# Kernel tuning notes

Measured on AMD Instinct MI355X. Metric: run time of the kernel, lower is better.

## Reference

```python
import jax, jax.numpy as jnp
import numpy as np

NUM_GROUPS = 32
EPS = 1e-6


def group_norm(x, gamma, beta):
    # x: (B, C, H, W), 32 groups, eps=1e-6, affine
    B, C, H, W = x.shape
    xg = x.reshape(B, NUM_GROUPS, C // NUM_GROUPS, H, W)
    mean = xg.mean(axis=(2, 3, 4), keepdims=True)
    var = xg.var(axis=(2, 3, 4), keepdims=True)
    xn = ((xg - mean) * jax.lax.rsqrt(var + EPS)).reshape(B, C, H, W)
    return xn * gamma[None, :, None, None] + beta[None, :, None, None]


def conv1x1(x, w, b):
    # 1x1 conv == channel matmul. x: (B,C,H,W), w: (O,C), b: (O,)
    return jnp.einsum('bchw,oc->bohw', x, w) + b[None, :, None, None]


def setup_inputs() -> dict:
    key = jax.random.key(0)
    B, C, H, W = 16, 512, 32, 32
    ks = jax.random.split(key, 12)
    s = 1.0 / np.sqrt(C)
    return {
        'x': jax.random.normal(ks[0], (B, C, H, W), dtype=jnp.float32),
        'gn_gamma': jnp.ones((C,), dtype=jnp.float32),
        'gn_beta': jnp.zeros((C,), dtype=jnp.float32),
        'wq': jax.random.normal(ks[1], (C, C), dtype=jnp.float32) * s,
        'bq': jnp.zeros((C,), dtype=jnp.float32),
        'wk': jax.random.normal(ks[2], (C, C), dtype=jnp.float32) * s,
        'bk': jnp.zeros((C,), dtype=jnp.float32),
        'wv': jax.random.normal(ks[3], (C, C), dtype=jnp.float32) * s,
        'bv': jnp.zeros((C,), dtype=jnp.float32),
        'wp': jax.random.normal(ks[4], (C, C), dtype=jnp.float32) * s,
        'bp': jnp.zeros((C,), dtype=jnp.float32),
    }


def reference(x, gn_gamma, gn_beta, wq, bq, wk, bk, wv, bv, wp, bp):
    B, C, H, W = x.shape
    residual = x
    xn = group_norm(x, gn_gamma, gn_beta)
    q = conv1x1(xn, wq, bq).reshape(B, C, H * W)  # (B, C, HW)
    k = conv1x1(xn, wk, bk).reshape(B, C, H * W)
    v = conv1x1(xn, wv, bv).reshape(B, C, H * W)
    scale = C ** (-0.5)
    # energy[b,i,j] = q_i . k_j
    energy = jnp.einsum('bci,bcj->bij', q, k) * scale
    attn = jax.nn.softmax(energy, axis=-1)
    # out[b,c,i] = sum_j attn[b,i,j] * v[b,c,j]
    out = jnp.einsum('bij,bcj->bci', attn, v).reshape(B, C, H, W)
    out = conv1x1(out, wp, bp)
    return out + residual
```

## Files before the change

### kernel.cpp

```cpp
#include <hip/hip_runtime.h>
#include <hip/hip_bf16.h>

using bf16 = __hip_bfloat16;

typedef __attribute__((ext_vector_type(8))) __bf16 bf16x8;
typedef __attribute__((ext_vector_type(4))) float floatx4;

#define EPS 1e-6f

#define RAW_BARRIER()  asm volatile("s_barrier" ::: "memory")
#define WAIT_VM6()     asm volatile("s_waitcnt vmcnt(6)" ::: "memory")
#define WAIT_VM4()     asm volatile("s_waitcnt vmcnt(4)" ::: "memory")
#define WAIT_VM0()     asm volatile("s_waitcnt vmcnt(0)" ::: "memory")

__device__ __forceinline__ void load_lds16(const void* g, void* l) {
    __builtin_amdgcn_global_load_lds(
        (const __attribute__((address_space(1))) void*)g,
        (__attribute__((address_space(3))) void*)l, 16, 0, 0);
}

__device__ __forceinline__ void storeOut(float* p, float v) { *p = v; }
__device__ __forceinline__ void storeOut(bf16* p, float v) { *p = __float2bfloat16(v); }

template <int BM, int BIAS_MODE, int SCALE_EN, int RESID_EN, int EXP_MODE,
          int ROWDIV, int QKV, typename OutT>
__global__ __launch_bounds__(256, 2) void gemm_nt(
    const bf16* __restrict__ A, long long aStride, int lda,
    const bf16* __restrict__ B, long long bStride, int ldb,
    OutT* __restrict__ D, long long dStride, int ldd,
    bf16* __restrict__ vout, long long vStride,
    const float* __restrict__ bias,
    const float* __restrict__ resid, long long rStride, int ldr,
    float* __restrict__ rowsum, int rsStride,
    int K, float scale, int tpb, int gx)
{
    constexpr int MI = BM / 32;
    constexpr int NLA = BM / 64;
    constexpr int NL = NLA + 2;

    __shared__ bf16 As[2][BM * 32];
    __shared__ bf16 Bs[2][128 * 32];

    const unsigned chunk = gridDim.x >> 3;
    const unsigned glob  = (blockIdx.x & 7) * chunk + (blockIdx.x >> 3);
    const unsigned z  = glob / (unsigned)tpb;
    const unsigned t  = glob % (unsigned)tpb;
    const int m0 = (int)(t / (unsigned)gx) * BM;
    const int n0 = (int)(t % (unsigned)gx) << 7;

    const int tid  = threadIdx.x;
    const int lane = tid & 63;
    const int wave = tid >> 6;
    const int wm   = wave >> 1;
    const int wn   = wave & 1;

    const bf16* Ab = A + (size_t)z * aStride + (size_t)m0 * lda;
    const bf16* Bb = B + (size_t)z * bStride + (size_t)n0 * ldb;

    floatx4 acc[MI][4];
#pragma unroll
    for (int i = 0; i < MI; ++i)
#pragma unroll
        for (int j = 0; j < 4; ++j) acc[i][j] = (floatx4){0.f, 0.f, 0.f, 0.f};

    const int laneRow = lane & 15;
    const int laneKq  = lane >> 4;
    const int kqs16 = (laneKq ^ ((laneRow >> 1) & 3)) << 4;

    auto stage = [&](int kt) {
        const int k0 = kt << 5;
        char* Ad = (char*)As[kt & 1];
        char* Bd = (char*)Bs[kt & 1];
#pragma unroll
        for (int t4 = 0; t4 < NLA; ++t4) {
            const int idx = tid + t4 * 256;
            const int r  = idx >> 2;
            const int qs = (idx & 3) ^ ((idx >> 3) & 3);
            load_lds16(Ab + (size_t)r * lda + k0 + qs * 8, Ad + idx * 16);
        }
#pragma unroll
        for (int t4 = 0; t4 < 2; ++t4) {
            const int idx = tid + t4 * 256;
            const int r  = idx >> 2;
            const int qs = (idx & 3) ^ ((idx >> 3) & 3);
            load_lds16(Bb + (size_t)r * ldb + k0 + qs * 8, Bd + idx * 16);
        }
    };

    const int kIters = K >> 5;
    stage(0);
    stage(1);
    for (int kt = 0; kt < kIters; ++kt) {
        if (kt + 1 < kIters) {
            if (NL == 6) { WAIT_VM6(); } else { WAIT_VM4(); }
        } else {
            WAIT_VM0();
        }
        RAW_BARRIER();

        const char* AsB = (const char*)As[kt & 1];
        const char* BsB = (const char*)Bs[kt & 1];
        bf16x8 af[MI], bfr[4];
#pragma unroll
        for (int im = 0; im < MI; ++im) {
            const int arow = wm * (BM / 2) + im * 16 + laneRow;
            af[im] = *(const bf16x8*)(AsB + arow * 64 + kqs16);
        }
#pragma unroll
        for (int in = 0; in < 4; ++in) {
            const int brow = wn * 64 + in * 16 + laneRow;
            bfr[in] = *(const bf16x8*)(BsB + brow * 64 + kqs16);
        }
#pragma unroll
        for (int im = 0; im < MI; ++im)
#pragma unroll
            for (int in = 0; in < 4; ++in)
                acc[im][in] = __builtin_amdgcn_mfma_f32_16x16x32_bf16(
                    af[im], bfr[in], acc[im][in], 0, 0, 0);

        RAW_BARRIER();
        if (kt + 2 < kIters) stage(kt + 2);
    }

    const size_t dbase = (size_t)z * dStride;
#pragma unroll
    for (int im = 0; im < MI; ++im) {
        const int gmb = m0 + wm * (BM / 2) + im * 16 + (laneKq << 2);
        float ri[4];
        if (ROWDIV) {
#pragma unroll
            for (int r = 0; r < 4; ++r)
                ri[r] = 1.f / rowsum[(size_t)z * rsStride + gmb + r];
        }
        float rsum[4] = {0.f, 0.f, 0.f, 0.f};
#pragma unroll
        for (int in = 0; in < 4; ++in) {
            const int gn = n0 + wn * 64 + in * 16 + laneRow;
            float bn = 0.f;
            if (BIAS_MODE == 2) bn = bias[gn];
            if (QKV && n0 >= 1024) {
                union { bf16 h[4]; ushort4 u; } pk;
#pragma unroll
                for (int r = 0; r < 4; ++r)
                    pk.h[r] = __float2bfloat16(acc[im][in][r] + bn);
                *(ushort4*)(vout + (size_t)z * vStride +
                            (size_t)(gn - 1024) * 1024 + gmb) = pk.u;
            } else {
#pragma unroll
                for (int r = 0; r < 4; ++r) {
                    const int gm = gmb + r;
                    float v = acc[im][in][r];
                    if (SCALE_EN) v *= scale;
                    if (EXP_MODE) { v = __expf(v); rsum[r] += v; }
                    if (ROWDIV) v *= ri[r];
                    if (BIAS_MODE == 1) v += bias[gm];
                    if (BIAS_MODE == 2) v += bn;
                    if (RESID_EN)
                        v += resid[(size_t)z * rStride + (size_t)gm * ldr + gn];
                    storeOut(D + dbase + (size_t)gm * ldd + gn, v);
                }
            }
        }
        if (EXP_MODE) {
#pragma unroll
            for (int r = 0; r < 4; ++r) {
                float s = rsum[r];
                s += __shfl_xor(s, 1);
                s += __shfl_xor(s, 2);
                s += __shfl_xor(s, 4);
                s += __shfl_xor(s, 8);
                if (laneRow == 0)
                    atomicAdd(rowsum + (size_t)z * rsStride + gmb + r, s);
            }
        }
    }
}

__global__ __launch_bounds__(256) void gn_stats(const float* __restrict__ x,
                                                float* __restrict__ stats)
{
    const int bg = blockIdx.x;
    const float4* p = (const float4*)(x + (size_t)bg * 16384);
    float s = 0.f, ss = 0.f;
    for (int i = threadIdx.x; i < 4096; i += 256) {
        float4 v = p[i];
        s  += v.x + v.y + v.z + v.w;
        ss += v.x * v.x + v.y * v.y + v.z * v.z + v.w * v.w;
    }
#pragma unroll
    for (int off = 32; off; off >>= 1) {
        s  += __shfl_down(s, off);
        ss += __shfl_down(ss, off);
    }
    __shared__ float rs[4], rss[4];
    const int wv = threadIdx.x >> 6;
    if ((threadIdx.x & 63) == 0) { rs[wv] = s; rss[wv] = ss; }
    __syncthreads();
    if (threadIdx.x == 0) {
        float S  = rs[0] + rs[1] + rs[2] + rs[3];
        float SS = rss[0] + rss[1] + rss[2] + rss[3];
        float mean = S * (1.f / 16384.f);
        float var  = SS * (1.f / 16384.f) - mean * mean;
        stats[2 * bg]     = mean;
        stats[2 * bg + 1] = rsqrtf(var + EPS);
    }
}

__global__ __launch_bounds__(256) void gn_apply_t(const float* __restrict__ x,
                                                  const float* __restrict__ stats,
                                                  const float* __restrict__ gamma,
                                                  const float* __restrict__ beta,
                                                  bf16* __restrict__ xnT)
{
    __shared__ bf16 tile[32][36];
    const int b = blockIdx.z, c0 = blockIdx.y * 32, i0 = blockIdx.x * 32;
    {
        const int cc = threadIdx.x >> 3;
        const int i4 = (threadIdx.x & 7) << 2;
        const int c  = c0 + cc;
        const float mean = stats[2 * ((b << 5) + (c >> 4))];
        const float rstd = stats[2 * ((b << 5) + (c >> 4)) + 1];
        const float a  = gamma[c] * rstd;
        const float bb = beta[c] - mean * a;
        float4 v = *(const float4*)(x + (((size_t)(b * 512 + c)) << 10) + i0 + i4);
        tile[cc][i4 + 0] = __float2bfloat16(v.x * a + bb);
        tile[cc][i4 + 1] = __float2bfloat16(v.y * a + bb);
        tile[cc][i4 + 2] = __float2bfloat16(v.z * a + bb);
        tile[cc][i4 + 3] = __float2bfloat16(v.w * a + bb);
    }
    __syncthreads();
    {
        const int ii = threadIdx.x >> 3;
        const int c4 = (threadIdx.x & 7) << 2;
        union { bf16 h[4]; uint2 u; } pk;
        pk.h[0] = tile[c4 + 0][ii];
        pk.h[1] = tile[c4 + 1][ii];
        pk.h[2] = tile[c4 + 2][ii];
        pk.h[3] = tile[c4 + 3][ii];
        *((uint2*)(xnT + (((size_t)(b * 1024 + i0 + ii)) << 9) + c0 + c4)) = pk.u;
    }
}

__global__ __launch_bounds__(256) void prep(
    const float* __restrict__ wq, const float* __restrict__ wk,
    const float* __restrict__ wv, const float* __restrict__ wp,
    bf16* __restrict__ wqkvb, bf16* __restrict__ wpb,
    const float* __restrict__ bq, const float* __restrict__ bk,
    const float* __restrict__ bv, float* __restrict__ bqkv,
    float* __restrict__ rowsum)
{
    const int id = blockIdx.x;
    if (id < 1024) {
        const int w = id >> 8;
        const float* src = (w == 0) ? wq : (w == 1) ? wk : (w == 2) ? wv : wp;
        bf16* dst = (w < 3) ? (wqkvb + (size_t)w * 262144) : wpb;
        const int g = (id & 255) * 256 + threadIdx.x;
        float4 v = ((const float4*)src)[g];
        union { bf16 h[4]; uint2 u; } pk;
        pk.h[0] = __float2bfloat16(v.x);
        pk.h[1] = __float2bfloat16(v.y);
        pk.h[2] = __float2bfloat16(v.z);
        pk.h[3] = __float2bfloat16(v.w);
        ((uint2*)dst)[g] = pk.u;
    } else if (id == 1024) {
        for (int t = threadIdx.x; t < 1536; t += 256)
            bqkv[t] = (t < 512) ? bq[t] : (t < 1024) ? bk[t - 512] : bv[t - 1024];
    } else {
        float4 zero = {0.f, 0.f, 0.f, 0.f};
#pragma unroll
        for (int j = 0; j < 16; ++j)
            ((float4*)rowsum)[threadIdx.x + j * 256] = zero;
    }
}

extern "C" void kernel_launch(void* const* d_in, const int* in_sizes, int n_in,
                              void* d_out, int out_size, void* d_ws, size_t ws_size,
                              hipStream_t stream)
{
    const float* x     = (const float*)d_in[0];
    const float* gamma = (const float*)d_in[1];
    const float* beta  = (const float*)d_in[2];
    const float* wq    = (const float*)d_in[3];
    const float* bq    = (const float*)d_in[4];
    const float* wk    = (const float*)d_in[5];
    const float* bk    = (const float*)d_in[6];
    const float* wv    = (const float*)d_in[7];
    const float* bv    = (const float*)d_in[8];
    const float* wp    = (const float*)d_in[9];
    const float* bp    = (const float*)d_in[10];
    float* out = (float*)d_out;

    char* ws = (char*)d_ws;
    size_t off = 0;
    auto alloc = [&](size_t bytes) -> char* {
        char* p = ws + off;
        off += (bytes + 255) & ~(size_t)255;
        return p;
    };

    const long long S  = 1024, C = 512;
    const long long BS = S * C;
    const long long ES = S * S;

    float* stats  = (float*)alloc(512 * 2 * sizeof(float));
    float* bqkv   = (float*)alloc(1536 * sizeof(float));
    float* rowsum = (float*)alloc((size_t)16 * S * sizeof(float));
    bf16* wqkvb = (bf16*)alloc((size_t)3 * C * C * 2);
    bf16* wpb   = (bf16*)alloc((size_t)C * C * 2);
    bf16* xnT   = (bf16*)alloc((size_t)16 * BS * 2);
    bf16* qkT   = (bf16*)alloc((size_t)16 * ES * 2);
    bf16* vv    = (bf16*)alloc((size_t)16 * BS * 2);
    bf16* O2    = (bf16*)alloc((size_t)16 * BS * 2);

    int CB = 16;
    while (CB > 1 && off + (size_t)CB * ES * 2 + 1024 > ws_size) CB >>= 1;
    bf16* P = (bf16*)alloc((size_t)CB * ES * 2);

    prep<<<1026, 256, 0, stream>>>(wq, wk, wv, wp, wqkvb, wpb, bq, bk, bv,
                                   bqkv, rowsum);

    gn_stats<<<512, 256, 0, stream>>>(x, stats);
    gn_apply_t<<<dim3(32, 16, 16), 256, 0, stream>>>(x, stats, gamma, beta, xnT);

    gemm_nt<256, 2, 0, 0, 0, 0, 1, bf16><<<768, 256, 0, stream>>>(
        xnT, BS, 512, wqkvb, 0, 512, qkT, ES, 1024, vv, BS,
        bqkv, nullptr, 0, 0, nullptr, 0, 512, 1.f, 48, 12);

    const float scale = 0.044194173824159216f;
    for (int b0 = 0; b0 < 16; b0 += CB) {
        gemm_nt<256, 0, 1, 0, 1, 0, 0, bf16><<<CB * 32, 256, 0, stream>>>(
            qkT + (size_t)b0 * ES, ES, 1024,
            qkT + (size_t)b0 * ES + 512, ES, 1024,
            P, ES, 1024, nullptr, 0,
            nullptr, nullptr, 0, 0, rowsum + (size_t)b0 * S, (int)S,
            512, scale, 32, 8);
        gemm_nt<128, 0, 0, 0, 0, 1, 0, bf16><<<CB * 32, 256, 0, stream>>>(
            P, ES, 1024,
            vv + (size_t)b0 * BS, BS, 1024,
            O2 + (size_t)b0 * BS, BS, 512, nullptr, 0,
            nullptr, nullptr, 0, 0, rowsum + (size_t)b0 * S, (int)S,
            1024, 1.f, 32, 4);
    }

    gemm_nt<128, 1, 0, 1, 0, 0, 0, float><<<512, 256, 0, stream>>>(
        wpb, 0, 512, O2, BS, 512, out, BS, 1024, nullptr, 0,
        bp, x, BS, 1024, nullptr, 0, 512, 1.f, 32, 8);
}
```

Measured before the change: 239.0 us.

## Rewrite GEMMs as 8-wave 256-row tiles with split-K LDS pipeline and setprio

Replaces the 4-wave GEMM with an 8-wave kernel using 256xBN tiles (BN = 256 or 128) and a BK=64 step split into two 32-wide halves. It uses dynamic LDS, double buffering and fine-grained vmcnt waits, and interleaves the staging of the next halves between MFMA clusters. MFMA bursts are wrapped with s_setprio so waves issuing math take priority over those issuing loads. The aim is more data reuse per block and better overlap of global-to-LDS loads with MFMA. The cost is much larger LDS use (up to 128 KB per block), fewer blocks on the grid and more barriers.

```diff
diff --git a/kernel.cpp b/kernel.cpp
--- a/kernel.cpp
+++ b/kernel.cpp
@@ -9,9 +9,13 @@
 #define EPS 1e-6f
 
 #define RAW_BARRIER()  asm volatile("s_barrier" ::: "memory")
+#define WAIT_VM8()     asm volatile("s_waitcnt vmcnt(8)" ::: "memory")
 #define WAIT_VM6()     asm volatile("s_waitcnt vmcnt(6)" ::: "memory")
 #define WAIT_VM4()     asm volatile("s_waitcnt vmcnt(4)" ::: "memory")
+#define WAIT_VM3()     asm volatile("s_waitcnt vmcnt(3)" ::: "memory")
 #define WAIT_VM0()     asm volatile("s_waitcnt vmcnt(0)" ::: "memory")
+#define PRIO1()        __builtin_amdgcn_s_setprio(1)
+#define PRIO0()        __builtin_amdgcn_s_setprio(0)
 
 __device__ __forceinline__ void load_lds16(const void* g, void* l) {
     __builtin_amdgcn_global_load_lds(
@@ -22,9 +26,11 @@
 __device__ __forceinline__ void storeOut(float* p, float v) { *p = v; }
 __device__ __forceinline__ void storeOut(bf16* p, float v) { *p = __float2bfloat16(v); }
 
-template <int BM, int BIAS_MODE, int SCALE_EN, int RESID_EN, int EXP_MODE,
+#define MFMA16(a, b, c) __builtin_amdgcn_mfma_f32_16x16x32_bf16(a, b, c, 0, 0, 0)
+
+template <int NI, int BIAS_MODE, int SCALE_EN, int RESID_EN, int EXP_MODE,
           int ROWDIV, int QKV, typename OutT>
-__global__ __launch_bounds__(256, 2) void gemm_nt(
+__global__ __launch_bounds__(512, 2) void gemm8(
     const bf16* __restrict__ A, long long aStride, int lda,
     const bf16* __restrict__ B, long long bStride, int ldb,
     OutT* __restrict__ D, long long dStride, int ldd,
@@ -34,98 +40,183 @@
     float* __restrict__ rowsum, int rsStride,
     int K, float scale, int tpb, int gx)
 {
-    constexpr int MI = BM / 32;
-    constexpr int NLA = BM / 64;
-    constexpr int NL = NLA + 2;
-
-    __shared__ bf16 As[2][BM * 32];
-    __shared__ bf16 Bs[2][128 * 32];
+    constexpr int BN  = NI * 64;
+    constexpr int ABH = 16384;
+    constexpr int BBH = BN * 64;
+    extern __shared__ char smem[];
 
     const unsigned chunk = gridDim.x >> 3;
     const unsigned glob  = (blockIdx.x & 7) * chunk + (blockIdx.x >> 3);
     const unsigned z  = glob / (unsigned)tpb;
     const unsigned t  = glob % (unsigned)tpb;
-    const int m0 = (int)(t / (unsigned)gx) * BM;
-    const int n0 = (int)(t % (unsigned)gx) << 7;
+    const int m0 = (int)(t / (unsigned)gx) << 8;
+    const int n0 = (int)(t % (unsigned)gx) * BN;
 
     const int tid  = threadIdx.x;
     const int lane = tid & 63;
     const int wave = tid >> 6;
-    const int wm   = wave >> 1;
-    const int wn   = wave & 1;
+    const int wm   = wave >> 2;
+    const int wn   = wave & 3;
 
     const bf16* Ab = A + (size_t)z * aStride + (size_t)m0 * lda;
     const bf16* Bb = B + (size_t)z * bStride + (size_t)n0 * ldb;
 
-    floatx4 acc[MI][4];
-#pragma unroll
-    for (int i = 0; i < MI; ++i)
-#pragma unroll
-        for (int j = 0; j < 4; ++j) acc[i][j] = (floatx4){0.f, 0.f, 0.f, 0.f};
+    floatx4 acc[8][NI];
+#pragma unroll
+    for (int i = 0; i < 8; ++i)
+#pragma unroll
+        for (int j = 0; j < NI; ++j) acc[i][j] = (floatx4){0.f, 0.f, 0.f, 0.f};
 
     const int laneRow = lane & 15;
     const int laneKq  = lane >> 4;
-    const int kqs16 = (laneKq ^ ((laneRow >> 1) & 3)) << 4;
-
-    auto stage = [&](int kt) {
-        const int k0 = kt << 5;
-        char* Ad = (char*)As[kt & 1];
-        char* Bd = (char*)Bs[kt & 1];
-#pragma unroll
-        for (int t4 = 0; t4 < NLA; ++t4) {
-            const int idx = tid + t4 * 256;
+    const int kqs16   = (laneKq ^ ((laneRow >> 1) & 3)) << 4;
+    const int arow0   = wm * 128 + laneRow;
+    const int brow0   = wn * (NI * 16) + laneRow;
+
+    auto stageA = [&](int kt, int h) {
+        char* dst = smem + ((kt & 1) * 2 + h) * ABH;
+        const int kb = (kt << 6) + (h << 5);
+#pragma unroll
+        for (int u = 0; u < 2; ++u) {
+            const int idx = tid + u * 512;
             const int r  = idx >> 2;
             const int qs = (idx & 3) ^ ((idx >> 3) & 3);
-            load_lds16(Ab + (size_t)r * lda + k0 + qs * 8, Ad + idx * 16);
-        }
-#pragma unroll
-        for (int t4 = 0; t4 < 2; ++t4) {
-            const int idx = tid + t4 * 256;
+            load_lds16(Ab + (size_t)r * lda + kb + qs * 8, dst + idx * 16);
+        }
+    };
+    auto stageB = [&](int kt, int h) {
+        char* dst = smem + 4 * ABH + ((kt & 1) * 2 + h) * BBH;
+        const int kb = (kt << 6) + (h << 5);
+        if constexpr (NI == 4) {
+#pragma unroll
+            for (int u = 0; u < 2; ++u) {
+                const int idx = tid + u * 512;
+                const int r  = idx >> 2;
+                const int qs = (idx & 3) ^ ((idx >> 3) & 3);
+                load_lds16(Bb + (size_t)r * ldb + kb + qs * 8, dst + idx * 16);
+            }
+        } else {
+            const int idx = tid;
             const int r  = idx >> 2;
             const int qs = (idx & 3) ^ ((idx >> 3) & 3);
-            load_lds16(Bb + (size_t)r * ldb + k0 + qs * 8, Bd + idx * 16);
+            load_lds16(Bb + (size_t)r * ldb + kb + qs * 8, dst + idx * 16);
         }
     };
 
-    const int kIters = K >> 5;
-    stage(0);
-    stage(1);
-    for (int kt = 0; kt < kIters; ++kt) {
-        if (kt + 1 < kIters) {
-            if (NL == 6) { WAIT_VM6(); } else { WAIT_VM4(); }
+    const int nt = K >> 6;
+    stageA(0, 0); stageB(0, 0); stageA(0, 1); stageB(0, 1);
+    stageA(1, 0); stageB(1, 0);
+
+    for (int kt = 0; kt < nt; ++kt) {
+        const char* Ablk = smem + (kt & 1) * 2 * ABH;
+        const char* Bblk = smem + 4 * ABH + (kt & 1) * 2 * BBH;
+        const bool lastT = (kt == nt - 1);
+
+        if (lastT) { if constexpr (NI == 4) WAIT_VM4(); else WAIT_VM3(); }
+        else       { if constexpr (NI == 4) WAIT_VM8(); else WAIT_VM6(); }
+        RAW_BARRIER();
+
+        if constexpr (NI == 4) {
+            bf16x8 af[4], bfr[4];
+#pragma unroll
+            for (int im = 0; im < 4; ++im)
+                af[im] = *(const bf16x8*)(Ablk + (arow0 + im * 16) * 64 + kqs16);
+#pragma unroll
+            for (int in = 0; in < 4; ++in)
+                bfr[in] = *(const bf16x8*)(Bblk + (brow0 + in * 16) * 64 + kqs16);
+            if (kt + 1 < nt) stageA(kt + 1, 1);
+            RAW_BARRIER();
+            PRIO1();
+#pragma unroll
+            for (int im = 0; im < 4; ++im)
+#pragma unroll
+                for (int in = 0; in < 4; ++in)
+                    acc[im][in] = MFMA16(af[im], bfr[in], acc[im][in]);
+            PRIO0();
+            RAW_BARRIER();
+#pragma unroll
+            for (int im = 0; im < 4; ++im)
+                af[im] = *(const bf16x8*)(Ablk + (arow0 + (im + 4) * 16) * 64 + kqs16);
+            if (kt + 1 < nt) stageB(kt + 1, 1);
+            RAW_BARRIER();
+            PRIO1();
+#pragma unroll
+            for (int im = 0; im < 4; ++im)
+#pragma unroll
+                for (int in = 0; in < 4; ++in)
+                    acc[im + 4][in] = MFMA16(af[im], bfr[in], acc[im + 4][in]);
+            PRIO0();
+            if (lastT) WAIT_VM0(); else WAIT_VM8();
+            RAW_BARRIER();
+#pragma unroll
+            for (int im = 0; im < 4; ++im)
+                af[im] = *(const bf16x8*)(Ablk + ABH + (arow0 + im * 16) * 64 + kqs16);
+#pragma unroll
+            for (int in = 0; in < 4; ++in)
+                bfr[in] = *(const bf16x8*)(Bblk + BBH + (brow0 + in * 16) * 64 + kqs16);
+            if (kt + 2 < nt) stageA(kt + 2, 0);
+            RAW_BARRIER();
+            PRIO1();
+#pragma unroll
+            for (int im = 0; im < 4; ++im)
+#pragma unroll
+                for (int in = 0; in < 4; ++in)
+                    acc[im][in] = MFMA16(af[im], bfr[in], acc[im][in]);
+            PRIO0();
+            RAW_BARRIER();
+#pragma unroll
+            for (int im = 0; im < 4; ++im)
+                af[im] = *(const bf16x8*)(Ablk + ABH + (arow0 + (im + 4) * 16) * 64 + kqs16);
+            if (kt + 2 < nt) stageB(kt + 2, 0);
+            RAW_BARRIER();
+            PRIO1();
+#pragma unroll
+            for (int im = 0; im < 4; ++im)
+#pragma unroll
+                for (int in = 0; in < 4; ++in)
+                    acc[im + 4][in] = MFMA16(af[im], bfr[in], acc[im + 4][in]);
+            PRIO0();
         } else {
-            WAIT_VM0();
-        }
-        RAW_BARRIER();
-
-        const char* AsB = (const char*)As[kt & 1];
-        const char* BsB = (const char*)Bs[kt & 1];
-        bf16x8 af[MI], bfr[4];
-#pragma unroll
-        for (int im = 0; im < MI; ++im) {
-            const int arow = wm * (BM / 2) + im * 16 + laneRow;
-            af[im] = *(const bf16x8*)(AsB + arow * 64 + kqs16);
-        }
-#pragma unroll
-        for (int in = 0; in < 4; ++in) {
-            const int brow = wn * 64 + in * 16 + laneRow;
-            bfr[in] = *(const bf16x8*)(BsB + brow * 64 + kqs16);
-        }
-#pragma unroll
-        for (int im = 0; im < MI; ++im)
-#pragma unroll
-            for (int in = 0; in < 4; ++in)
-                acc[im][in] = __builtin_amdgcn_mfma_f32_16x16x32_bf16(
-                    af[im], bfr[in], acc[im][in], 0, 0, 0);
-
-        RAW_BARRIER();
-        if (kt + 2 < kIters) stage(kt + 2);
+            bf16x8 af[8], bfr[2];
+#pragma unroll
+            for (int im = 0; im < 8; ++im)
+                af[im] = *(const bf16x8*)(Ablk + (arow0 + im * 16) * 64 + kqs16);
+#pragma unroll
+            for (int in = 0; in < 2; ++in)
+                bfr[in] = *(const bf16x8*)(Bblk + (brow0 + in * 16) * 64 + kqs16);
+            if (kt + 1 < nt) { stageA(kt + 1, 1); stageB(kt + 1, 1); }
+            RAW_BARRIER();
+            PRIO1();
+#pragma unroll
+            for (int im = 0; im < 8; ++im)
+#pragma unroll
+                for (int in = 0; in < 2; ++in)
+                    acc[im][in] = MFMA16(af[im], bfr[in], acc[im][in]);
+            PRIO0();
+            if (lastT) WAIT_VM0(); else WAIT_VM6();
+            RAW_BARRIER();
+#pragma unroll
+            for (int im = 0; im < 8; ++im)
+                af[im] = *(const bf16x8*)(Ablk + ABH + (arow0 + im * 16) * 64 + kqs16);
+#pragma unroll
+            for (int in = 0; in < 2; ++in)
+                bfr[in] = *(const bf16x8*)(Bblk + BBH + (brow0 + in * 16) * 64 + kqs16);
+            if (kt + 2 < nt) { stageA(kt + 2, 0); stageB(kt + 2, 0); }
+            RAW_BARRIER();
+            PRIO1();
+#pragma unroll
+            for (int im = 0; im < 8; ++im)
+#pragma unroll
+                for (int in = 0; in < 2; ++in)
+                    acc[im][in] = MFMA16(af[im], bfr[in], acc[im][in]);
+            PRIO0();
+        }
     }
 
     const size_t dbase = (size_t)z * dStride;
 #pragma unroll
-    for (int im = 0; im < MI; ++im) {
-        const int gmb = m0 + wm * (BM / 2) + im * 16 + (laneKq << 2);
+    for (int im = 0; im < 8; ++im) {
+        const int gmb = m0 + wm * 128 + im * 16 + (laneKq << 2);
         float ri[4];
         if (ROWDIV) {
 #pragma unroll
@@ -134,8 +225,8 @@
         }
         float rsum[4] = {0.f, 0.f, 0.f, 0.f};
 #pragma unroll
-        for (int in = 0; in < 4; ++in) {
-            const int gn = n0 + wn * 64 + in * 16 + laneRow;
+        for (int in = 0; in < NI; ++in) {
+            const int gn = n0 + wn * (NI * 16) + in * 16 + laneRow;
             float bn = 0.f;
             if (BIAS_MODE == 2) bn = bias[gn];
             if (QKV && n0 >= 1024) {
@@ -316,33 +407,42 @@
     while (CB > 1 && off + (size_t)CB * ES * 2 + 1024 > ws_size) CB >>= 1;
     bf16* P = (bf16*)alloc((size_t)CB * ES * 2);
 
+    hipFuncSetAttribute((const void*)gemm8<4, 2, 0, 0, 0, 0, 1, bf16>,
+                        hipFuncAttributeMaxDynamicSharedMemorySize, 131072);
+    hipFuncSetAttribute((const void*)gemm8<4, 0, 1, 0, 1, 0, 0, bf16>,
+                        hipFuncAttributeMaxDynamicSharedMemorySize, 131072);
+    hipFuncSetAttribute((const void*)gemm8<2, 0, 0, 0, 0, 1, 0, bf16>,
+                        hipFuncAttributeMaxDynamicSharedMemorySize, 98304);
+    hipFuncSetAttribute((const void*)gemm8<2, 1, 0, 1, 0, 0, 0, float>,
+                        hipFuncAttributeMaxDynamicSharedMemorySize, 98304);
+
     prep<<<1026, 256, 0, stream>>>(wq, wk, wv, wp, wqkvb, wpb, bq, bk, bv,
                                    bqkv, rowsum);
 
     gn_stats<<<512, 256, 0, stream>>>(x, stats);
     gn_apply_t<<<dim3(32, 16, 16), 256, 0, stream>>>(x, stats, gamma, beta, xnT);
 
-    gemm_nt<256, 2, 0, 0, 0, 0, 1, bf16><<<768, 256, 0, stream>>>(
+    gemm8<4, 2, 0, 0, 0, 0, 1, bf16><<<384, 512, 131072, stream>>>(
         xnT, BS, 512, wqkvb, 0, 512, qkT, ES, 1024, vv, BS,
-        bqkv, nullptr, 0, 0, nullptr, 0, 512, 1.f, 48, 12);
+        bqkv, nullptr, 0, 0, nullptr, 0, 512, 1.f, 24, 6);
 
     const float scale = 0.044194173824159216f;
     for (int b0 = 0; b0 < 16; b0 += CB) {
-        gemm_nt<256, 0, 1, 0, 1, 0, 0, bf16><<<CB * 32, 256, 0, stream>>>(
+        gemm8<4, 0, 1, 0, 1, 0, 0, bf16><<<CB * 16, 512, 131072, stream>>>(
             qkT + (size_t)b0 * ES, ES, 1024,
             qkT + (size_t)b0 * ES + 512, ES, 1024,
             P, ES, 1024, nullptr, 0,
             nullptr, nullptr, 0, 0, rowsum + (size_t)b0 * S, (int)S,
-            512, scale, 32, 8);
-        gemm_nt<128, 0, 0, 0, 0, 1, 0, bf16><<<CB * 32, 256, 0, stream>>>(
+            512, scale, 16, 4);
+        gemm8<2, 0, 0, 0, 0, 1, 0, bf16><<<CB * 16, 512, 98304, stream>>>(
             P, ES, 1024,
             vv + (size_t)b0 * BS, BS, 1024,
             O2 + (size_t)b0 * BS, BS, 512, nullptr, 0,
             nullptr, nullptr, 0, 0, rowsum + (size_t)b0 * S, (int)S,
-            1024, 1.f, 32, 4);
-    }
-
-    gemm_nt<128, 1, 0, 1, 0, 0, 0, float><<<512, 256, 0, stream>>>(
+            1024, 1.f, 16, 4);
+    }
+
+    gemm8<2, 1, 0, 1, 0, 0, 0, float><<<256, 512, 98304, stream>>>(
         wpb, 0, 512, O2, BS, 512, out, BS, 1024, nullptr, 0,
-        bp, x, BS, 1024, nullptr, 0, 512, 1.f, 32, 8);
-}
+        bp, x, BS, 1024, nullptr, 0, 512, 1.f, 16, 8);
+}
```

Result: faster. 229.6 us (-3.9%).

## Restructure GEMM into 128x128 tiles with split-half K pipeline and priority hints

Applied to the files above, without the earlier changes.

Replaces the templated BM GEMM with a fixed 128x128 tile kernel. Each 64-wide K step is split into two 32-wide halves held in dynamic shared memory, and loads for later halves are issued between the half-steps so memory traffic overlaps the MFMA work. MFMA sections are wrapped in s_setprio to favour the compute waves. Grid sizes for the QKV and QK^T launches double because BM drops from 256 to 128, giving more blocks at the cost of less A-tile reuse per block. Each kernel now uses 64KB of LDS, which may limit occupancy to two blocks per CU.

```diff
diff --git a/kernel.cpp b/kernel.cpp
--- a/kernel.cpp
+++ b/kernel.cpp
@@ -9,9 +9,11 @@
 #define EPS 1e-6f
 
 #define RAW_BARRIER()  asm volatile("s_barrier" ::: "memory")
-#define WAIT_VM6()     asm volatile("s_waitcnt vmcnt(6)" ::: "memory")
+#define WAIT_VM8()     asm volatile("s_waitcnt vmcnt(8)" ::: "memory")
 #define WAIT_VM4()     asm volatile("s_waitcnt vmcnt(4)" ::: "memory")
 #define WAIT_VM0()     asm volatile("s_waitcnt vmcnt(0)" ::: "memory")
+#define PRIO1()        __builtin_amdgcn_s_setprio(1)
+#define PRIO0()        __builtin_amdgcn_s_setprio(0)
 
 __device__ __forceinline__ void load_lds16(const void* g, void* l) {
     __builtin_amdgcn_global_load_lds(
@@ -22,9 +24,11 @@
 __device__ __forceinline__ void storeOut(float* p, float v) { *p = v; }
 __device__ __forceinline__ void storeOut(bf16* p, float v) { *p = __float2bfloat16(v); }
 
-template <int BM, int BIAS_MODE, int SCALE_EN, int RESID_EN, int EXP_MODE,
+#define MFMA16(a, b, c) __builtin_amdgcn_mfma_f32_16x16x32_bf16(a, b, c, 0, 0, 0)
+
+template <int BIAS_MODE, int SCALE_EN, int RESID_EN, int EXP_MODE,
           int ROWDIV, int QKV, typename OutT>
-__global__ __launch_bounds__(256, 2) void gemm_nt(
+__global__ __launch_bounds__(256, 2) void gemm2b(
     const bf16* __restrict__ A, long long aStride, int lda,
     const bf16* __restrict__ B, long long bStride, int ldb,
     OutT* __restrict__ D, long long dStride, int ldd,
@@ -34,18 +38,14 @@
     float* __restrict__ rowsum, int rsStride,
     int K, float scale, int tpb, int gx)
 {
-    constexpr int MI = BM / 32;
-    constexpr int NLA = BM / 64;
-    constexpr int NL = NLA + 2;
-
-    __shared__ bf16 As[2][BM * 32];
-    __shared__ bf16 Bs[2][128 * 32];
+    constexpr int HB = 8192;
+    extern __shared__ char smem[];
 
     const unsigned chunk = gridDim.x >> 3;
     const unsigned glob  = (blockIdx.x & 7) * chunk + (blockIdx.x >> 3);
     const unsigned z  = glob / (unsigned)tpb;
     const unsigned t  = glob % (unsigned)tpb;
-    const int m0 = (int)(t / (unsigned)gx) * BM;
+    const int m0 = (int)(t / (unsigned)gx) << 7;
     const int n0 = (int)(t % (unsigned)gx) << 7;
 
     const int tid  = threadIdx.x;
@@ -57,75 +57,88 @@
     const bf16* Ab = A + (size_t)z * aStride + (size_t)m0 * lda;
     const bf16* Bb = B + (size_t)z * bStride + (size_t)n0 * ldb;
 
-    floatx4 acc[MI][4];
-#pragma unroll
-    for (int i = 0; i < MI; ++i)
+    floatx4 acc[4][4];
+#pragma unroll
+    for (int i = 0; i < 4; ++i)
 #pragma unroll
         for (int j = 0; j < 4; ++j) acc[i][j] = (floatx4){0.f, 0.f, 0.f, 0.f};
 
     const int laneRow = lane & 15;
     const int laneKq  = lane >> 4;
-    const int kqs16 = (laneKq ^ ((laneRow >> 1) & 3)) << 4;
-
-    auto stage = [&](int kt) {
-        const int k0 = kt << 5;
-        char* Ad = (char*)As[kt & 1];
-        char* Bd = (char*)Bs[kt & 1];
-#pragma unroll
-        for (int t4 = 0; t4 < NLA; ++t4) {
-            const int idx = tid + t4 * 256;
+    const int kqs16   = (laneKq ^ ((laneRow >> 1) & 3)) << 4;
+    const int arow0   = wm * 64 + laneRow;
+    const int brow0   = wn * 64 + laneRow;
+
+    auto stage = [&](int kt, int h) {
+        char* Adst = smem + ((kt & 1) * 2 + h) * HB;
+        char* Bdst = smem + 4 * HB + ((kt & 1) * 2 + h) * HB;
+        const int kb = (kt << 6) + (h << 5);
+#pragma unroll
+        for (int u = 0; u < 2; ++u) {
+            const int idx = tid + u * 256;
             const int r  = idx >> 2;
             const int qs = (idx & 3) ^ ((idx >> 3) & 3);
-            load_lds16(Ab + (size_t)r * lda + k0 + qs * 8, Ad + idx * 16);
-        }
-#pragma unroll
-        for (int t4 = 0; t4 < 2; ++t4) {
-            const int idx = tid + t4 * 256;
+            load_lds16(Ab + (size_t)r * lda + kb + qs * 8, Adst + idx * 16);
+        }
+#pragma unroll
+        for (int u = 0; u < 2; ++u) {
+            const int idx = tid + u * 256;
             const int r  = idx >> 2;
             const int qs = (idx & 3) ^ ((idx >> 3) & 3);
-            load_lds16(Bb + (size_t)r * ldb + k0 + qs * 8, Bd + idx * 16);
+            load_lds16(Bb + (size_t)r * ldb + kb + qs * 8, Bdst + idx * 16);
         }
     };
 
-    const int kIters = K >> 5;
-    stage(0);
-    stage(1);
-    for (int kt = 0; kt < kIters; ++kt) {
-        if (kt + 1 < kIters) {
-            if (NL == 6) { WAIT_VM6(); } else { WAIT_VM4(); }
-        } else {
-            WAIT_VM0();
-        }
+    const int nt = K >> 6;
+    stage(0, 0); stage(0, 1); stage(1, 0);
+
+    for (int kt = 0; kt < nt; ++kt) {
+        const char* Ablk = smem + (kt & 1) * 2 * HB;
+        const char* Bblk = smem + 4 * HB + (kt & 1) * 2 * HB;
+        const bool lastT = (kt == nt - 1);
+
+        if (lastT) WAIT_VM4(); else WAIT_VM8();
         RAW_BARRIER();
-
-        const char* AsB = (const char*)As[kt & 1];
-        const char* BsB = (const char*)Bs[kt & 1];
-        bf16x8 af[MI], bfr[4];
-#pragma unroll
-        for (int im = 0; im < MI; ++im) {
-            const int arow = wm * (BM / 2) + im * 16 + laneRow;
-            af[im] = *(const bf16x8*)(AsB + arow * 64 + kqs16);
-        }
-#pragma unroll
-        for (int in = 0; in < 4; ++in) {
-            const int brow = wn * 64 + in * 16 + laneRow;
-            bfr[in] = *(const bf16x8*)(BsB + brow * 64 + kqs16);
-        }
-#pragma unroll
-        for (int im = 0; im < MI; ++im)
+        bf16x8 af[4], bfr[4];
+#pragma unroll
+        for (int im = 0; im < 4; ++im)
+            af[im] = *(const bf16x8*)(Ablk + (arow0 + im * 16) * 64 + kqs16);
+#pragma unroll
+        for (int in = 0; in < 4; ++in)
+            bfr[in] = *(const bf16x8*)(Bblk + (brow0 + in * 16) * 64 + kqs16);
+        if (kt + 1 < nt) stage(kt + 1, 1);
+        RAW_BARRIER();
+        PRIO1();
+#pragma unroll
+        for (int im = 0; im < 4; ++im)
 #pragma unroll
             for (int in = 0; in < 4; ++in)
-                acc[im][in] = __builtin_amdgcn_mfma_f32_16x16x32_bf16(
-                    af[im], bfr[in], acc[im][in], 0, 0, 0);
-
+                acc[im][in] = MFMA16(af[im], bfr[in], acc[im][in]);
+        PRIO0();
+
+        if (lastT) WAIT_VM0(); else WAIT_VM8();
         RAW_BARRIER();
-        if (kt + 2 < kIters) stage(kt + 2);
+#pragma unroll
+        for (int im = 0; im < 4; ++im)
+            af[im] = *(const bf16x8*)(Ablk + HB + (arow0 + im * 16) * 64 + kqs16);
+#pragma unroll
+        for (int in = 0; in < 4; ++in)
+            bfr[in] = *(const bf16x8*)(Bblk + HB + (brow0 + in * 16) * 64 + kqs16);
+        if (kt + 2 < nt) stage(kt + 2, 0);
+        RAW_BARRIER();
+        PRIO1();
+#pragma unroll
+        for (int im = 0; im < 4; ++im)
+#pragma unroll
+            for (int in = 0; in < 4; ++in)
+                acc[im][in] = MFMA16(af[im], bfr[in], acc[im][in]);
+        PRIO0();
     }
 
     const size_t dbase = (size_t)z * dStride;
 #pragma unroll
-    for (int im = 0; im < MI; ++im) {
-        const int gmb = m0 + wm * (BM / 2) + im * 16 + (laneKq << 2);
+    for (int im = 0; im < 4; ++im) {
+        const int gmb = m0 + wm * 64 + im * 16 + (laneKq << 2);
         float ri[4];
         if (ROWDIV) {
 #pragma unroll
@@ -316,25 +329,34 @@
     while (CB > 1 && off + (size_t)CB * ES * 2 + 1024 > ws_size) CB >>= 1;
     bf16* P = (bf16*)alloc((size_t)CB * ES * 2);
 
+    hipFuncSetAttribute((const void*)gemm2b<2, 0, 0, 0, 0, 1, bf16>,
+                        hipFuncAttributeMaxDynamicSharedMemorySize, 65536);
+    hipFuncSetAttribute((const void*)gemm2b<0, 1, 0, 1, 0, 0, bf16>,
+                        hipFuncAttributeMaxDynamicSharedMemorySize, 65536);
+    hipFuncSetAttribute((const void*)gemm2b<0, 0, 0, 0, 1, 0, bf16>,
+                        hipFuncAttributeMaxDynamicSharedMemorySize, 65536);
+    hipFuncSetAttribute((const void*)gemm2b<1, 0, 1, 0, 0, 0, float>,
+                        hipFuncAttributeMaxDynamicSharedMemorySize, 65536);
+
     prep<<<1026, 256, 0, stream>>>(wq, wk, wv, wp, wqkvb, wpb, bq, bk, bv,
                                    bqkv, rowsum);
 
     gn_stats<<<512, 256, 0, stream>>>(x, stats);
     gn_apply_t<<<dim3(32, 16, 16), 256, 0, stream>>>(x, stats, gamma, beta, xnT);
 
-    gemm_nt<256, 2, 0, 0, 0, 0, 1, bf16><<<768, 256, 0, stream>>>(
+    gemm2b<2, 0, 0, 0, 0, 1, bf16><<<1536, 256, 65536, stream>>>(
         xnT, BS, 512, wqkvb, 0, 512, qkT, ES, 1024, vv, BS,
-        bqkv, nullptr, 0, 0, nullptr, 0, 512, 1.f, 48, 12);
+        bqkv, nullptr, 0, 0, nullptr, 0, 512, 1.f, 96, 12);
 
     const float scale = 0.044194173824159216f;
     for (int b0 = 0; b0 < 16; b0 += CB) {
-        gemm_nt<256, 0, 1, 0, 1, 0, 0, bf16><<<CB * 32, 256, 0, stream>>>(
+        gemm2b<0, 1, 0, 1, 0, 0, bf16><<<CB * 64, 256, 65536, stream>>>(
             qkT + (size_t)b0 * ES, ES, 1024,
             qkT + (size_t)b0 * ES + 512, ES, 1024,
             P, ES, 1024, nullptr, 0,
             nullptr, nullptr, 0, 0, rowsum + (size_t)b0 * S, (int)S,
-            512, scale, 32, 8);
-        gemm_nt<128, 0, 0, 0, 0, 1, 0, bf16><<<CB * 32, 256, 0, stream>>>(
+            512, scale, 64, 8);
+        gemm2b<0, 0, 0, 0, 1, 0, bf16><<<CB * 32, 256, 65536, stream>>>(
             P, ES, 1024,
             vv + (size_t)b0 * BS, BS, 1024,
             O2 + (size_t)b0 * BS, BS, 512, nullptr, 0,
@@ -342,7 +364,7 @@
             1024, 1.f, 32, 4);
     }
 
-    gemm_nt<128, 1, 0, 1, 0, 0, 0, float><<<512, 256, 0, stream>>>(
+    gemm2b<1, 0, 1, 0, 0, 0, float><<<512, 256, 65536, stream>>>(
         wpb, 0, 512, O2, BS, 512, out, BS, 1024, nullptr, 0,
         bp, x, BS, 1024, nullptr, 0, 512, 1.f, 32, 8);
 }
```

Measured after the change: 224.9 us, median of 2. -5.9%, faster.
